# Kernel tuning notes

Hardware: AMD Instinct MI355X
Metric: run time of the kernel (lower is better)

## Reference

```python
import jax, jax.numpy as jnp
import numpy as np

B, C, H, W = 16, 512, 32, 32
MID = max(8, C // 4)      # gate hidden
CA_MID = max(8, C // 4)   # channel-attn hidden
LOW_RADIUS = 0.35


def dct_mat(N):
    # Orthonormal DCT-II matrix: D[k,n] = s_k * sqrt(2/N) * cos(pi*(2n+1)*k/(2N))
    k = jnp.arange(N, dtype=jnp.float32)[:, None]
    n = jnp.arange(N, dtype=jnp.float32)[None, :]
    M = jnp.cos(jnp.pi * (2.0 * n + 1.0) * k / (2.0 * N)) * jnp.sqrt(2.0 / N)
    return M.at[0].multiply(1.0 / jnp.sqrt(2.0))


def build_low_mask(Hh, Ww, low_radius):
    yy = jnp.arange(Hh, dtype=jnp.float32)[:, None] / max(Hh - 1, 1)
    xx = jnp.arange(Ww, dtype=jnp.float32)[None, :] / max(Ww - 1, 1)
    rr = jnp.sqrt(yy ** 2 + xx ** 2)
    rr = rr / jnp.maximum(rr.max(), 1e-6)
    return (rr <= low_radius).astype(jnp.float32)[None, None]  # [1,1,H,W]


def conv1x1(x, w, b):
    # x: [B,Cin,H,W], w: [Cout,Cin], b: [Cout]
    return jnp.einsum('bchw,oc->bohw', x, w) + b[None, :, None, None]


def freq_transform(x, gw1, gb1, gw2, gb2, Dh, Dw, lm):
    # gate: avgpool -> 1x1 -> relu -> 1x1 -> sigmoid, output 2 scalars per sample
    pooled = jnp.mean(x, axis=(2, 3), keepdims=True)  # [B,C,1,1]
    g = jax.nn.sigmoid(conv1x1(jax.nn.relu(conv1x1(pooled, gw1, gb1)), gw2, gb2))
    g_low, g_high = g[:, 0:1], g[:, 1:2]  # [B,1,1,1]
    # 2D ortho DCT: Dh @ x @ Dw^T
    freq = jnp.einsum('ih,bchw->bciw', Dh, x)
    freq = jnp.einsum('jw,bchw->bchj', Dw, freq)
    # frequency gating fused
    gated = freq * (g_low * lm + g_high * (1.0 - lm))
    # inverse: Dh^T @ freq @ Dw
    out = jnp.einsum('hi,bchw->bciw', Dh, gated)
    out = jnp.einsum('wj,bchw->bchj', Dw, out)
    return out


def setup_inputs() -> dict:
    key = jax.random.key(0)
    ks = jax.random.split(key, 24)
    s = 1.0 / np.sqrt(C)
    d = {
        'rgb': jax.random.normal(ks[0], (B, C, H, W), jnp.float32),
        'dsm': jax.random.normal(ks[1], (B, C, H, W), jnp.float32),
        'rgb_w': jax.random.normal(ks[2], (C, C), jnp.float32) * s,
        'rgb_b': jax.random.normal(ks[3], (C,), jnp.float32) * 0.01,
        'dsm_w': jax.random.normal(ks[4], (C, C), jnp.float32) * s,
        'dsm_b': jax.random.normal(ks[5], (C,), jnp.float32) * 0.01,
        'gate_w1': jax.random.normal(ks[6], (MID, C), jnp.float32) * s,
        'gate_b1': jax.random.normal(ks[7], (MID,), jnp.float32) * 0.01,
        'gate_w2': jax.random.normal(ks[8], (2, MID), jnp.float32) * (1.0 / np.sqrt(MID)),
        'gate_b2': jax.random.normal(ks[9], (2,), jnp.float32) * 0.01,
        'q_w': jax.random.normal(ks[10], (C, C), jnp.float32) * s,
        'q_b': jax.random.normal(ks[11], (C,), jnp.float32) * 0.01,
        'k_w': jax.random.normal(ks[12], (C, C), jnp.float32) * s,
        'k_b': jax.random.normal(ks[13], (C,), jnp.float32) * 0.01,
        'v_w': jax.random.normal(ks[14], (C, C), jnp.float32) * s,
        'v_b': jax.random.normal(ks[15], (C,), jnp.float32) * 0.01,
        'sp_w': jax.random.normal(ks[16], (C, C, 3, 3), jnp.float32) * (s / 3.0),
        'sp_b': jax.random.normal(ks[17], (C,), jnp.float32) * 0.01,
        'ca_w1': jax.random.normal(ks[18], (CA_MID, C), jnp.float32) * s,
        'ca_b1': jax.random.normal(ks[19], (CA_MID,), jnp.float32) * 0.01,
        'ca_w2': jax.random.normal(ks[20], (C, CA_MID), jnp.float32) * (1.0 / np.sqrt(CA_MID)),
        'ca_b2': jax.random.normal(ks[21], (C,), jnp.float32) * 0.01,
    }
    return d


def reference(rgb, dsm, rgb_w, rgb_b, dsm_w, dsm_b, gate_w1, gate_b1, gate_w2, gate_b2,
              q_w, q_b, k_w, k_b, v_w, v_b, sp_w, sp_b, ca_w1, ca_b1, ca_w2, ca_b2):
    Dh, Dw = dct_mat(H), dct_mat(W)
    lm = build_low_mask(H, W, LOW_RADIUS)

    rgb_p = conv1x1(rgb, rgb_w, rgb_b)
    dsm_p = conv1x1(dsm, dsm_w, dsm_b)

    rgb_f = freq_transform(rgb_p, gate_w1, gate_b1, gate_w2, gate_b2, Dh, Dw, lm)
    dsm_f = freq_transform(dsm_p, gate_w1, gate_b1, gate_w2, gate_b2, Dh, Dw, lm)

    q = conv1x1(rgb_f, q_w, q_b).reshape(B, C, H * W)
    k = conv1x1(dsm_f, k_w, k_b).reshape(B, C, H * W)
    v = conv1x1(dsm_f, v_w, v_b).reshape(B, C, H * W)

    # attn over spatial tokens: [B,N,N]
    scores = jnp.einsum('bcn,bcm->bnm', q, k) / jnp.sqrt(jnp.float32(C))
    attn = jax.nn.softmax(scores, axis=-1)
    out = jnp.einsum('bnm,bcm->bcn', attn, v).reshape(B, C, H, W)

    spatial = jax.lax.conv_general_dilated(
        out, sp_w, window_strides=(1, 1), padding='SAME',
        dimension_numbers=('NCHW', 'OIHW', 'NCHW')) + sp_b[None, :, None, None]

    pooled = jnp.mean(spatial, axis=(2, 3), keepdims=True)
    weight = jax.nn.sigmoid(conv1x1(jax.nn.relu(conv1x1(pooled, ca_w1, ca_b1)), ca_w2, ca_b2))
    return rgb_p + spatial * weight
```

## Files before the change

### kernel.cpp

```cpp
#include <hip/hip_runtime.h>

typedef long long i64;
typedef unsigned int u32;
typedef unsigned short u16;

#define Bq 16
#define Cq 512
#define Hq 32
#define Wq 32
#define Nq 1024
#define MIDq 128
#define XPBq 591872

typedef __attribute__((ext_vector_type(8))) short bf16x8;
typedef __attribute__((ext_vector_type(4))) float f32x4;

static __device__ __forceinline__ u16 f2bf(float f) {
  u32 u = __float_as_uint(f);
  u = (u + 0x7FFFu + ((u >> 16) & 1u)) >> 16;
  return (u16)u;
}
static __device__ __forceinline__ float bf2f(u16 h) {
  return __uint_as_float(((u32)h) << 16);
}

__global__ __launch_bounds__(256) void k_prep(
    const float* __restrict__ rgb_w, const float* __restrict__ dsm_w,
    const float* __restrict__ q_w, const float* __restrict__ k_w,
    const float* __restrict__ v_w, const float* __restrict__ sp_w,
    u16* __restrict__ rw_h, u16* __restrict__ rw_l,
    u16* __restrict__ dw_h, u16* __restrict__ dw_l,
    u16* __restrict__ qw_h, u16* __restrict__ qw_l,
    u16* __restrict__ kw_h, u16* __restrict__ kw_l,
    u16* __restrict__ vw_h, u16* __restrict__ vw_l,
    u16* __restrict__ w9h, u16* __restrict__ w9l,
    float* __restrict__ Dm, float* __restrict__ lm) {
  int blk = blockIdx.x, tid = threadIdx.x;
  if (blk < 1280) {
    int wi = blk >> 8;
    const float* src = wi == 0 ? rgb_w : wi == 1 ? dsm_w : wi == 2 ? q_w : wi == 3 ? k_w : v_w;
    u16* hi = wi == 0 ? rw_h : wi == 1 ? dw_h : wi == 2 ? qw_h : wi == 3 ? kw_h : vw_h;
    u16* lo = wi == 0 ? rw_l : wi == 1 ? dw_l : wi == 2 ? qw_l : wi == 3 ? kw_l : vw_l;
    i64 idx = ((i64)(blk & 255) * 256 + tid) * 4;
    float4 f = *(const float4*)(src + idx);
    ushort4 h, l;
    h.x = f2bf(f.x); l.x = f2bf(f.x - bf2f(h.x));
    h.y = f2bf(f.y); l.y = f2bf(f.y - bf2f(h.y));
    h.z = f2bf(f.z); l.z = f2bf(f.z - bf2f(h.z));
    h.w = f2bf(f.w); l.w = f2bf(f.w - bf2f(h.w));
    *(ushort4*)(hi + idx) = h;
    *(ushort4*)(lo + idx) = l;
  } else if (blk < 1536) {
    int idx = (blk - 1280) * 256 + tid;
    int o = idx >> 7;
    int c4 = (idx & 127) << 2;
    float vals[4][9];
#pragma unroll
    for (int j = 0; j < 4; j++) {
      const float* wp = sp_w + ((i64)o * Cq + c4 + j) * 9;
#pragma unroll
      for (int t = 0; t < 9; t++) vals[j][t] = wp[t];
    }
#pragma unroll
    for (int t = 0; t < 9; t++) {
      ushort4 h, l;
      h.x = f2bf(vals[0][t]); l.x = f2bf(vals[0][t] - bf2f(h.x));
      h.y = f2bf(vals[1][t]); l.y = f2bf(vals[1][t] - bf2f(h.y));
      h.z = f2bf(vals[2][t]); l.z = f2bf(vals[2][t] - bf2f(h.z));
      h.w = f2bf(vals[3][t]); l.w = f2bf(vals[3][t] - bf2f(h.w));
      i64 od = (i64)t * (Cq * Cq) + (i64)o * Cq + c4;
      *(ushort4*)(w9h + od) = h;
      *(ushort4*)(w9l + od) = l;
    }
  } else {
#pragma unroll
    for (int q4 = 0; q4 < 4; q4++) {
      int t = tid * 4 + q4;
      int i = t >> 5, j = t & 31;
      float v = cosf(3.14159265358979323846f * (2.0f * j + 1.0f) * (float)i / 64.0f) * 0.25f;
      if (i == 0) v *= 0.7071067811865476f;
      Dm[t] = v;
      float yy = i * (1.0f / 31.0f), xx = j * (1.0f / 31.0f);
      float rr = sqrtf(yy * yy + xx * xx) * 0.7071067811865476f;
      lm[t] = (rr <= 0.35f) ? 1.0f : 0.0f;
    }
  }
}

__global__ __launch_bounds__(64) void k_zero_border(u16* __restrict__ xp) {
  int i = blockIdx.x;
  int b = blockIdx.y;
  int arr = blockIdx.z;
  int pr;
  if (i < 34) pr = i;
  else if (i < 68) pr = 33 * 34 + (i - 34);
  else { int j = i - 68; pr = (1 + (j >> 1)) * 34 + (j & 1) * 33; }
  u16* p = xp + (i64)arr * ((i64)Bq * XPBq) + (i64)b * XPBq + (i64)pr * Cq;
  *(uint4*)(p + threadIdx.x * 8) = (uint4){0u, 0u, 0u, 0u};
}

__global__ __launch_bounds__(256) void k_gemm(
    const u16* __restrict__ Ahi, const u16* __restrict__ Alo,
    const float* __restrict__ Af32, int a_mode, i64 sAb,
    const u16* __restrict__ Bhi, const u16* __restrict__ Blo,
    const float* __restrict__ Bf32, int b_mode, i64 sBb,
    const float* __restrict__ bias, int bias_mode, float scale,
    int M, int N, int K,
    float* __restrict__ Cf, u16* __restrict__ Chi, u16* __restrict__ Clo,
    i64 sCb, int out_mode) {
  __shared__ __align__(16) u16 As_h[128][40];
  __shared__ __align__(16) u16 As_l[128][40];
  __shared__ __align__(16) u16 Bs_h[128][40];
  __shared__ __align__(16) u16 Bs_l[128][40];
  int tid = threadIdx.x;
  int gx = gridDim.x, gxy = gx * gridDim.y;
  int nwg = gxy * gridDim.z;
  int orig = blockIdx.x + gx * blockIdx.y + gxy * blockIdx.z;
  int wg = (nwg & 7) ? orig : ((orig & 7) * (nwg >> 3) + (orig >> 3));
  int b = wg / gxy;
  int rem = wg - b * gxy;
  int m0 = (rem / gx) << 7;
  int n0 = (rem - (rem / gx) * gx) << 7;
  const u16* pAhi = Ahi + (i64)b * (a_mode ? 0 : sAb);
  const u16* pAlo = Alo + (i64)b * (a_mode ? 0 : sAb);
  const float* pAf = a_mode ? (Af32 + (i64)b * sAb) : nullptr;
  const u16* pBhi = Bhi + (i64)b * (b_mode ? 0 : sBb);
  const u16* pBlo = Blo + (i64)b * (b_mode ? 0 : sBb);
  const float* pBf = b_mode ? (Bf32 + (i64)b * sBb) : nullptr;
  int lane = tid & 63;
  int wid = tid >> 6;
  int wm = (wid & 1) << 6;
  int wn = (wid >> 1) << 6;
  int l15 = lane & 15;
  int g8 = (lane >> 4) << 3;
  f32x4 acc[4][4];
#pragma unroll
  for (int mi = 0; mi < 4; mi++)
#pragma unroll
    for (int nj = 0; nj < 4; nj++)
      acc[mi][nj] = (f32x4){0.f, 0.f, 0.f, 0.f};

  for (int k0 = 0; k0 < K; k0 += 32) {
    if (a_mode == 0) {
#pragma unroll
      for (int i = 0; i < 4; i++) {
        int r = ((i & 1) << 6) + (tid >> 2);
        int seg = tid & 3;
        const u16* src = (i < 2) ? pAhi : pAlo;
        uint4 val = *(const uint4*)(src + (i64)(m0 + r) * K + k0 + seg * 8);
        if (i < 2) *(uint4*)&As_h[r][seg * 8] = val;
        else       *(uint4*)&As_l[r][seg * 8] = val;
      }
    } else {
      int cs = tid >> 6, ns = tid & 63;
      const float* src = pAf + (i64)(k0 + cs * 8) * M + m0 + ns * 2;
      float2 f[8];
#pragma unroll
      for (int j = 0; j < 8; j++) f[j] = *(const float2*)(src + (i64)j * M);
#pragma unroll
      for (int i = 0; i < 2; i++) {
        union { u16 u[8]; uint4 v; } hh, ll;
#pragma unroll
        for (int j = 0; j < 8; j++) {
          float x = i ? f[j].y : f[j].x;
          u16 h = f2bf(x);
          hh.u[j] = h;
          ll.u[j] = (u16)(__float_as_uint(x - bf2f(h)) >> 16);
        }
        *(uint4*)&As_h[2 * ns + i][8 * cs] = hh.v;
        *(uint4*)&As_l[2 * ns + i][8 * cs] = ll.v;
      }
    }
    if (b_mode == 0) {
#pragma unroll
      for (int i = 0; i < 4; i++) {
        int r = ((i & 1) << 6) + (tid >> 2);
        int seg = tid & 3;
        const u16* src = (i < 2) ? pBhi : pBlo;
        uint4 val = *(const uint4*)(src + (i64)(n0 + r) * K + k0 + seg * 8);
        if (i < 2) *(uint4*)&Bs_h[r][seg * 8] = val;
        else       *(uint4*)&Bs_l[r][seg * 8] = val;
      }
    } else {
      int cs = tid >> 6, ns = tid & 63;
      const float* src = pBf + (i64)(k0 + cs * 8) * N + n0 + ns * 2;
      float2 f[8];
#pragma unroll
      for (int j = 0; j < 8; j++) f[j] = *(const float2*)(src + (i64)j * N);
#pragma unroll
      for (int i = 0; i < 2; i++) {
        union { u16 u[8]; uint4 v; } hh, ll;
#pragma unroll
        for (int j = 0; j < 8; j++) {
          float x = i ? f[j].y : f[j].x;
          u16 h = f2bf(x);
          hh.u[j] = h;
          ll.u[j] = (u16)(__float_as_uint(x - bf2f(h)) >> 16);
        }
        *(uint4*)&Bs_h[2 * ns + i][8 * cs] = hh.v;
        *(uint4*)&Bs_l[2 * ns + i][8 * cs] = ll.v;
      }
    }
    __syncthreads();
    bf16x8 ah[4], al[4], bh[4], bl[4];
#pragma unroll
    for (int mi = 0; mi < 4; mi++) {
      int row = wm + mi * 16 + l15;
      ah[mi] = *(const bf16x8*)&As_h[row][g8];
      al[mi] = *(const bf16x8*)&As_l[row][g8];
    }
#pragma unroll
    for (int nj = 0; nj < 4; nj++) {
      int row = wn + nj * 16 + l15;
      bh[nj] = *(const bf16x8*)&Bs_h[row][g8];
      bl[nj] = *(const bf16x8*)&Bs_l[row][g8];
    }
#pragma unroll
    for (int mi = 0; mi < 4; mi++)
#pragma unroll
      for (int nj = 0; nj < 4; nj++) {
        acc[mi][nj] = __builtin_amdgcn_mfma_f32_16x16x32_bf16(ah[mi], bh[nj], acc[mi][nj], 0, 0, 0);
        acc[mi][nj] = __builtin_amdgcn_mfma_f32_16x16x32_bf16(ah[mi], bl[nj], acc[mi][nj], 0, 0, 0);
        acc[mi][nj] = __builtin_amdgcn_mfma_f32_16x16x32_bf16(al[mi], bh[nj], acc[mi][nj], 0, 0, 0);
      }
    __syncthreads();
  }

#pragma unroll
  for (int mi = 0; mi < 4; mi++)
#pragma unroll
    for (int nj = 0; nj < 4; nj++) {
      int col_g = n0 + wn + nj * 16 + l15;
      int row_b = m0 + wm + mi * 16 + ((lane >> 4) << 2);
      float v4[4];
#pragma unroll
      for (int r = 0; r < 4; r++) {
        float val = acc[mi][nj][r] * scale;
        if (bias_mode == 1) val += bias[row_b + r];
        else if (bias_mode == 2) val += bias[col_g];
        v4[r] = val;
      }
      if (out_mode == 0) {
#pragma unroll
        for (int r = 0; r < 4; r++)
          Cf[(i64)b * sCb + (i64)(row_b + r) * N + col_g] = v4[r];
      } else if (out_mode == 1) {
#pragma unroll
        for (int r = 0; r < 4; r++) {
          i64 o = (i64)b * sCb + (i64)(row_b + r) * N + col_g;
          u16 h = f2bf(v4[r]);
          Chi[o] = h;
          Clo[o] = f2bf(v4[r] - bf2f(h));
        }
      } else {
        int pr = ((col_g >> 5) + 1) * 34 + (col_g & 31) + 1;
        i64 o = (i64)b * sCb + (i64)pr * Cq + row_b;
        ushort4 hh, ll;
        hh.x = f2bf(v4[0]); ll.x = f2bf(v4[0] - bf2f(hh.x));
        hh.y = f2bf(v4[1]); ll.y = f2bf(v4[1] - bf2f(hh.y));
        hh.z = f2bf(v4[2]); ll.z = f2bf(v4[2] - bf2f(hh.z));
        hh.w = f2bf(v4[3]); ll.w = f2bf(v4[3] - bf2f(hh.w));
        *(ushort4*)(Chi + o) = hh;
        *(ushort4*)(Clo + o) = ll;
      }
    }
}

__global__ __launch_bounds__(256) void k_conv3_mfma(
    const u16* __restrict__ Wh, const u16* __restrict__ Wl,
    const u16* __restrict__ Xh, const u16* __restrict__ Xl,
    const float* __restrict__ bias, float* __restrict__ out) {
  __shared__ __align__(16) u16 As_h[128][72];
  __shared__ __align__(16) u16 As_l[128][72];
  __shared__ __align__(16) u16 Bs_h[128][72];
  __shared__ __align__(16) u16 Bs_l[128][72];
  int tid = threadIdx.x;
  int gx = gridDim.x, gxy = gx * gridDim.y;
  int nwg = gxy * gridDim.z;
  int orig = blockIdx.x + gx * blockIdx.y + gxy * blockIdx.z;
  int wg = (nwg & 7) ? orig : ((orig & 7) * (nwg >> 3) + (orig >> 3));
  int b = wg / gxy;
  int rem = wg - b * gxy;
  int m0 = (rem / gx) << 7;
  int n0 = (rem - (rem / gx) * gx) << 7;
  const u16* pXh = Xh + (i64)b * XPBq;
  const u16* pXl = Xl + (i64)b * XPBq;
  int lane = tid & 63;
  int wid = tid >> 6;
  int wm = (wid & 1) << 6;
  int wn = (wid >> 1) << 6;
  int l15 = lane & 15;
  int g8 = (lane >> 4) << 3;
  int rr = tid >> 2, seg = tid & 3;
  int n_a = n0 + rr, n_b = n0 + 64 + rr;
  int prb0 = (n_a >> 5) * 34 + (n_a & 31);
  int prb1 = (n_b >> 5) * 34 + (n_b & 31);
  f32x4 acc[4][4];
#pragma unroll
  for (int mi = 0; mi < 4; mi++)
#pragma unroll
    for (int nj = 0; nj < 4; nj++)
      acc[mi][nj] = (f32x4){0.f, 0.f, 0.f, 0.f};

  for (int tap = 0; tap < 9; tap++) {
    int doff = (tap / 3) * 34 + (tap % 3);
    const u16* wth = Wh + (i64)tap * (Cq * Cq);
    const u16* wtl = Wl + (i64)tap * (Cq * Cq);
    i64 bb0 = (i64)(prb0 + doff) * Cq;
    i64 bb1 = (i64)(prb1 + doff) * Cq;
    for (int c0 = 0; c0 < Cq; c0 += 64) {
#pragma unroll
      for (int half = 0; half < 2; half++) {
        int col = seg * 8 + half * 32;
        i64 gc = c0 + col;
        *(uint4*)&As_h[rr][col]      = *(const uint4*)(wth + (i64)(m0 + rr) * Cq + gc);
        *(uint4*)&As_h[64 + rr][col] = *(const uint4*)(wth + (i64)(m0 + 64 + rr) * Cq + gc);
        *(uint4*)&As_l[rr][col]      = *(const uint4*)(wtl + (i64)(m0 + rr) * Cq + gc);
        *(uint4*)&As_l[64 + rr][col] = *(const uint4*)(wtl + (i64)(m0 + 64 + rr) * Cq + gc);
        *(uint4*)&Bs_h[rr][col]      = *(const uint4*)(pXh + bb0 + gc);
        *(uint4*)&Bs_h[64 + rr][col] = *(const uint4*)(pXh + bb1 + gc);
        *(uint4*)&Bs_l[rr][col]      = *(const uint4*)(pXl + bb0 + gc);
        *(uint4*)&Bs_l[64 + rr][col] = *(const uint4*)(pXl + bb1 + gc);
      }
      __syncthreads();
#pragma unroll
      for (int ks = 0; ks < 2; ks++) {
        int gk = ks * 32 + g8;
        bf16x8 ah[4], al[4], bh[4], bl[4];
#pragma unroll
        for (int mi = 0; mi < 4; mi++) {
          int row = wm + mi * 16 + l15;
          ah[mi] = *(const bf16x8*)&As_h[row][gk];
          al[mi] = *(const bf16x8*)&As_l[row][gk];
        }
#pragma unroll
        for (int nj = 0; nj < 4; nj++) {
          int row = wn + nj * 16 + l15;
          bh[nj] = *(const bf16x8*)&Bs_h[row][gk];
          bl[nj] = *(const bf16x8*)&Bs_l[row][gk];
        }
#pragma unroll
        for (int mi = 0; mi < 4; mi++)
#pragma unroll
          for (int nj = 0; nj < 4; nj++) {
            acc[mi][nj] = __builtin_amdgcn_mfma_f32_16x16x32_bf16(ah[mi], bh[nj], acc[mi][nj], 0, 0, 0);
            acc[mi][nj] = __builtin_amdgcn_mfma_f32_16x16x32_bf16(ah[mi], bl[nj], acc[mi][nj], 0, 0, 0);
            acc[mi][nj] = __builtin_amdgcn_mfma_f32_16x16x32_bf16(al[mi], bh[nj], acc[mi][nj], 0, 0, 0);
          }
      }
      __syncthreads();
    }
  }

#pragma unroll
  for (int mi = 0; mi < 4; mi++)
#pragma unroll
    for (int nj = 0; nj < 4; nj++) {
      int col_g = n0 + wn + nj * 16 + l15;
#pragma unroll
      for (int r = 0; r < 4; r++) {
        int row_g = m0 + wm + mi * 16 + ((lane >> 4) << 2) + r;
        float val = acc[mi][nj][r] + bias[row_g];
        out[(i64)b * (Cq * Nq) + (i64)row_g * Nq + col_g] = val;
      }
    }
}

__global__ __launch_bounds__(256) void k_pool(const float* __restrict__ x, float* __restrict__ o) {
  int gw = (int)((blockIdx.x * 256 + threadIdx.x) >> 6);
  int ln = threadIdx.x & 63;
  const float* p = x + (i64)gw * Nq;
  float s = 0.f;
#pragma unroll
  for (int it = 0; it < 4; it++) {
    float4 v = *(const float4*)(p + ln * 4 + it * 256);
    s += v.x + v.y + v.z + v.w;
  }
#pragma unroll
  for (int off = 32; off > 0; off >>= 1) s += __shfl_xor(s, off, 64);
  if (ln == 0) o[gw] = s * (1.0f / 1024.0f);
}

__global__ __launch_bounds__(128) void k_gate(
    const float* __restrict__ pooled, const float* __restrict__ w1,
    const float* __restrict__ b1, const float* __restrict__ w2,
    const float* __restrict__ b2, float* __restrict__ g) {
  __shared__ float pl[Cq];
  __shared__ float h[MIDq];
  int bb = blockIdx.x, tid = threadIdx.x;
  for (int c = tid; c < Cq; c += 128) pl[c] = pooled[bb * Cq + c];
  __syncthreads();
  float s = b1[tid];
  const float* wr = w1 + (i64)tid * Cq;
  for (int c = 0; c < Cq; c++) s = fmaf(wr[c], pl[c], s);
  h[tid] = fmaxf(s, 0.f);
  __syncthreads();
  if (tid < 2) {
    float t = b2[tid];
    const float* w2r = w2 + tid * MIDq;
    for (int m = 0; m < MIDq; m++) t = fmaf(w2r[m], h[m], t);
    g[bb * 2 + tid] = 1.0f / (1.0f + expf(-t));
  }
}

__global__ __launch_bounds__(256) void k_freq(
    const float* __restrict__ xr, const float* __restrict__ xd,
    float* __restrict__ yr, float* __restrict__ yd,
    const float* __restrict__ g_r, const float* __restrict__ g_d,
    const float* __restrict__ Dm, const float* __restrict__ lm) {
  __shared__ float Ds[32][36], Dt[32][36], Xs[32][36], T1[32][36];
  int bid = blockIdx.x;
  const float* x; float* y; const float* g;
  if (bid < Bq * Cq) {
    x = xr + (i64)bid * Nq; y = yr + (i64)bid * Nq; g = g_r + (bid >> 9) * 2;
  } else {
    int id = bid - Bq * Cq;
    x = xd + (i64)id * Nq; y = yd + (i64)id * Nq; g = g_d + (id >> 9) * 2;
  }
  int tid = threadIdx.x;
  int r_ = tid >> 3, j4 = (tid & 7) << 2;
  {
    float4 dv = *(const float4*)(Dm + tid * 4);
    *(float4*)&Ds[r_][j4] = dv;
    Dt[j4 + 0][r_] = dv.x; Dt[j4 + 1][r_] = dv.y;
    Dt[j4 + 2][r_] = dv.z; Dt[j4 + 3][r_] = dv.w;
    *(float4*)&Xs[r_][j4] = *(const float4*)(x + tid * 4);
  }
  float gl = g[0], gh = g[1];
  __syncthreads();
  float a0 = 0, a1 = 0, a2 = 0, a3 = 0;
#pragma unroll
  for (int h = 0; h < 32; h++) {
    float a = Ds[r_][h];
    float4 bv = *(const float4*)&Xs[h][j4];
    a0 = fmaf(a, bv.x, a0); a1 = fmaf(a, bv.y, a1);
    a2 = fmaf(a, bv.z, a2); a3 = fmaf(a, bv.w, a3);
  }
  *(float4*)&T1[r_][j4] = make_float4(a0, a1, a2, a3);
  __syncthreads();
  a0 = a1 = a2 = a3 = 0;
#pragma unroll
  for (int w = 0; w < 32; w++) {
    float a = T1[r_][w];
    float4 bv = *(const float4*)&Dt[w][j4];
    a0 = fmaf(a, bv.x, a0); a1 = fmaf(a, bv.y, a1);
    a2 = fmaf(a, bv.z, a2); a3 = fmaf(a, bv.w, a3);
  }
  {
    float4 mv = *(const float4*)(lm + r_ * 32 + j4);
    a0 *= fmaf(gl, mv.x, gh * (1.f - mv.x));
    a1 *= fmaf(gl, mv.y, gh * (1.f - mv.y));
    a2 *= fmaf(gl, mv.z, gh * (1.f - mv.z));
    a3 *= fmaf(gl, mv.w, gh * (1.f - mv.w));
  }
  __syncthreads();
  *(float4*)&Xs[r_][j4] = make_float4(a0, a1, a2, a3);
  __syncthreads();
  a0 = a1 = a2 = a3 = 0;
#pragma unroll
  for (int ii = 0; ii < 32; ii++) {
    float a = Dt[r_][ii];
    float4 bv = *(const float4*)&Xs[ii][j4];
    a0 = fmaf(a, bv.x, a0); a1 = fmaf(a, bv.y, a1);
    a2 = fmaf(a, bv.z, a2); a3 = fmaf(a, bv.w, a3);
  }
  __syncthreads();
  *(float4*)&T1[r_][j4] = make_float4(a0, a1, a2, a3);
  __syncthreads();
  a0 = a1 = a2 = a3 = 0;
#pragma unroll
  for (int jj = 0; jj < 32; jj++) {
    float a = T1[r_][jj];
    float4 bv = *(const float4*)&Ds[jj][j4];
    a0 = fmaf(a, bv.x, a0); a1 = fmaf(a, bv.y, a1);
    a2 = fmaf(a, bv.z, a2); a3 = fmaf(a, bv.w, a3);
  }
  *(float4*)(y + tid * 4) = make_float4(a0, a1, a2, a3);
}

__global__ __launch_bounds__(256) void k_softmax_split(
    const float* __restrict__ sc, u16* __restrict__ ahi, u16* __restrict__ alo) {
  __shared__ float redm[4], reds[4];
  i64 row = blockIdx.x;
  const float* p = sc + row * (i64)Nq;
  int tid = threadIdx.x;
  float4 v = ((const float4*)p)[tid];
  float mx = fmaxf(fmaxf(v.x, v.y), fmaxf(v.z, v.w));
#pragma unroll
  for (int o = 32; o > 0; o >>= 1) mx = fmaxf(mx, __shfl_xor(mx, o, 64));
  if ((tid & 63) == 0) redm[tid >> 6] = mx;
  __syncthreads();
  mx = fmaxf(fmaxf(redm[0], redm[1]), fmaxf(redm[2], redm[3]));
  v.x = expf(v.x - mx); v.y = expf(v.y - mx);
  v.z = expf(v.z - mx); v.w = expf(v.w - mx);
  float s = v.x + v.y + v.z + v.w;
#pragma unroll
  for (int o = 32; o > 0; o >>= 1) s += __shfl_xor(s, o, 64);
  if ((tid & 63) == 0) reds[tid >> 6] = s;
  __syncthreads();
  s = reds[0] + reds[1] + reds[2] + reds[3];
  float inv = 1.0f / s;
  v.x *= inv; v.y *= inv; v.z *= inv; v.w *= inv;
  ushort4 h, l;
  h.x = f2bf(v.x); l.x = f2bf(v.x - bf2f(h.x));
  h.y = f2bf(v.y); l.y = f2bf(v.y - bf2f(h.y));
  h.z = f2bf(v.z); l.z = f2bf(v.z - bf2f(h.z));
  h.w = f2bf(v.w); l.w = f2bf(v.w - bf2f(h.w));
  *(ushort4*)(ahi + row * Nq + tid * 4) = h;
  *(ushort4*)(alo + row * Nq + tid * 4) = l;
}

__global__ __launch_bounds__(512) void k_ca(
    const float* __restrict__ pooled, const float* __restrict__ w1,
    const float* __restrict__ b1, const float* __restrict__ w2,
    const float* __restrict__ b2, float* __restrict__ wt) {
  __shared__ float pl[Cq];
  __shared__ float h[MIDq];
  int b = blockIdx.x, tid = threadIdx.x;
  pl[tid] = pooled[b * Cq + tid];
  __syncthreads();
  if (tid < MIDq) {
    float s = b1[tid];
    const float* wr = w1 + (i64)tid * Cq;
    for (int c = 0; c < Cq; c++) s = fmaf(wr[c], pl[c], s);
    h[tid] = fmaxf(s, 0.f);
  }
  __syncthreads();
  float s = b2[tid];
  const float* wr = w2 + (i64)tid * MIDq;
  for (int m = 0; m < MIDq; m++) s = fmaf(wr[m], h[m], s);
  wt[b * Cq + tid] = 1.0f / (1.0f + expf(-s));
}

__global__ __launch_bounds__(256) void k_final(
    const float* __restrict__ rgbp, const float* __restrict__ sp,
    const float* __restrict__ wt, float* __restrict__ out) {
  i64 idx = (i64)blockIdx.x * 256 + threadIdx.x;
  float4 a = ((const float4*)rgbp)[idx];
  float4 s = ((const float4*)sp)[idx];
  float w = wt[idx >> 8];
  float4 r;
  r.x = fmaf(s.x, w, a.x); r.y = fmaf(s.y, w, a.y);
  r.z = fmaf(s.z, w, a.z); r.w = fmaf(s.w, w, a.w);
  ((float4*)out)[idx] = r;
}

extern "C" void kernel_launch(void* const* d_in, const int* in_sizes, int n_in,
                              void* d_out, int out_size, void* d_ws, size_t ws_size,
                              hipStream_t stream) {
  (void)in_sizes; (void)n_in; (void)out_size; (void)ws_size;
  const float* rgb    = (const float*)d_in[0];
  const float* dsm    = (const float*)d_in[1];
  const float* rgb_w  = (const float*)d_in[2];
  const float* rgb_b  = (const float*)d_in[3];
  const float* dsm_w  = (const float*)d_in[4];
  const float* dsm_b  = (const float*)d_in[5];
  const float* gate_w1 = (const float*)d_in[6];
  const float* gate_b1 = (const float*)d_in[7];
  const float* gate_w2 = (const float*)d_in[8];
  const float* gate_b2 = (const float*)d_in[9];
  const float* q_w = (const float*)d_in[10];
  const float* q_b = (const float*)d_in[11];
  const float* k_w = (const float*)d_in[12];
  const float* k_b = (const float*)d_in[13];
  const float* v_w = (const float*)d_in[14];
  const float* v_b = (const float*)d_in[15];
  const float* sp_w = (const float*)d_in[16];
  const float* sp_b = (const float*)d_in[17];
  const float* ca_w1 = (const float*)d_in[18];
  const float* ca_b1 = (const float*)d_in[19];
  const float* ca_w2 = (const float*)d_in[20];
  const float* ca_b2 = (const float*)d_in[21];

  const i64 S  = (i64)Bq * Cq * Nq;
  const i64 SU = S;
  const i64 WE = (i64)Cq * Cq;
  const i64 XPT = (i64)Bq * XPBq;

  float* wsf = (float*)d_ws;
  float* rgbp   = wsf;
  float* dsmp   = wsf + S;
  float* rgbf   = wsf + 2 * S;
  float* dsmf   = wsf + 3 * S;
  float* scores  = dsmp;
  float* spatial = dsmf;
  u16* XPh = (u16*)dsmp;
  u16* XPl = XPh + XPT;
  float* smallr = wsf + 4 * S;
  float* Dm     = smallr;
  float* lm     = smallr + 1024;
  float* pooled = smallr + 2048;
  float* g_all  = smallr + 18432;
  float* wt     = smallr + 18496;
  u16* ub = (u16*)(wsf + 4 * S + 32768);
  u16* U0 = ub;          u16* U1 = ub + SU;
  u16* U2 = ub + 2 * SU;
  u16* U4 = ub + 4 * SU; u16* U5 = ub + 5 * SU;
  u16* wb = ub + 6 * SU;
  u16* rgbw_h = wb;           u16* rgbw_l = wb + WE;
  u16* dsmw_h = wb + 2 * WE;  u16* dsmw_l = wb + 3 * WE;
  u16* qw_h   = wb + 4 * WE;  u16* qw_l   = wb + 5 * WE;
  u16* kw_h   = wb + 6 * WE;  u16* kw_l   = wb + 7 * WE;
  u16* vw_h   = wb + 8 * WE;  u16* vw_l   = wb + 9 * WE;
  u16* w9h    = wb + 10 * WE; u16* w9l    = wb + 19 * WE;

  const i64 sT = (i64)Nq * Cq;
  const i64 sS = (i64)Nq * Nq;
  const float rsqc = 0.044194173824159216f;

  k_prep<<<1537, 256, 0, stream>>>(rgb_w, dsm_w, q_w, k_w, v_w, sp_w,
                                   rgbw_h, rgbw_l, dsmw_h, dsmw_l, qw_h, qw_l,
                                   kw_h, kw_l, vw_h, vw_l, w9h, w9l, Dm, lm);

  dim3 gW(Nq / 128, Cq / 128, Bq);
  dim3 gQ(Cq / 128, Nq / 128, Bq);
  dim3 gS(Nq / 128, Nq / 128, Bq);

  k_gemm<<<gW, 256, 0, stream>>>(rgbw_h, rgbw_l, nullptr, 0, 0,
                                 nullptr, nullptr, rgb, 1, sT,
                                 rgb_b, 1, 1.0f, Cq, Nq, Cq,
                                 rgbp, nullptr, nullptr, sT, 0);
  k_gemm<<<gW, 256, 0, stream>>>(dsmw_h, dsmw_l, nullptr, 0, 0,
                                 nullptr, nullptr, dsm, 1, sT,
                                 dsm_b, 1, 1.0f, Cq, Nq, Cq,
                                 dsmp, nullptr, nullptr, sT, 0);

  k_pool<<<(2 * Bq * Cq) / 4, 256, 0, stream>>>(rgbp, pooled);
  k_gate<<<32, 128, 0, stream>>>(pooled, gate_w1, gate_b1, gate_w2, gate_b2, g_all);

  k_freq<<<2 * Bq * Cq, 256, 0, stream>>>(rgbp, dsmp, rgbf, dsmf, g_all, g_all + 32, Dm, lm);

  k_gemm<<<gQ, 256, 0, stream>>>(nullptr, nullptr, rgbf, 1, sT,
                                 qw_h, qw_l, nullptr, 0, 0,
                                 q_b, 2, 1.0f, Nq, Cq, Cq,
                                 nullptr, U4, U5, sT, 1);
  k_gemm<<<gQ, 256, 0, stream>>>(nullptr, nullptr, dsmf, 1, sT,
                                 kw_h, kw_l, nullptr, 0, 0,
                                 k_b, 2, 1.0f, Nq, Cq, Cq,
                                 nullptr, U0, U1, sT, 1);
  k_gemm<<<gS, 256, 0, stream>>>(U4, U5, nullptr, 0, sT,
                                 U0, U1, nullptr, 0, sT,
                                 nullptr, 0, rsqc, Nq, Nq, Cq,
                                 scores, nullptr, nullptr, sS, 0);
  k_gemm<<<gW, 256, 0, stream>>>(vw_h, vw_l, nullptr, 0, 0,
                                 nullptr, nullptr, dsmf, 1, sT,
                                 v_b, 1, 1.0f, Cq, Nq, Cq,
                                 nullptr, U4, U5, sT, 1);
  k_softmax_split<<<Bq * Nq, 256, 0, stream>>>(scores, U0, U2);
  k_zero_border<<<dim3(132, Bq, 2), 64, 0, stream>>>(XPh);
  k_gemm<<<gW, 256, 0, stream>>>(U4, U5, nullptr, 0, sT,
                                 U0, U2, nullptr, 0, sS,
                                 nullptr, 0, 1.0f, Cq, Nq, Nq,
                                 nullptr, XPh, XPl, XPBq, 2);

  k_conv3_mfma<<<dim3(Nq / 128, Cq / 128, Bq), 256, 0, stream>>>(
      w9h, w9l, XPh, XPl, sp_b, spatial);

  k_pool<<<(Bq * Cq) / 4, 256, 0, stream>>>(spatial, pooled);
  k_ca<<<Bq, 512, 0, stream>>>(pooled, ca_w1, ca_b1, ca_w2, ca_b2, wt);

  k_final<<<(int)(S / 4 / 256), 256, 0, stream>>>(rgbp, spatial, wt, (float*)d_out);
}
```

Baseline: 758.9 us.

## Reuse halo input tile across all nine conv taps in shared memory

The 3x3 conv GEMM now loads a padded halo block of input rows (6 padded image rows, 204 positions) into shared memory once per 32-channel chunk. It then iterates all nine taps by offsetting into that tile, instead of re-reading shifted input from global memory for every tap. This cuts global input traffic by about 9x at the cost of 2.6x more staged rows. The K chunk shrinks from 64 to 32, so there are more syncs per MFMA. The unpadded 32-wide LDS rows may also cause bank conflicts.

```diff
diff --git a/kernel.cpp b/kernel.cpp
--- a/kernel.cpp
+++ b/kernel.cpp
@@ -270,10 +270,10 @@
     const u16* __restrict__ Wh, const u16* __restrict__ Wl,
     const u16* __restrict__ Xh, const u16* __restrict__ Xl,
     const float* __restrict__ bias, float* __restrict__ out) {
-  __shared__ __align__(16) u16 As_h[128][72];
-  __shared__ __align__(16) u16 As_l[128][72];
-  __shared__ __align__(16) u16 Bs_h[128][72];
-  __shared__ __align__(16) u16 Bs_l[128][72];
+  __shared__ __align__(16) u16 As_h[128][32];
+  __shared__ __align__(16) u16 As_l[128][32];
+  __shared__ __align__(16) u16 Bs_h[204][32];
+  __shared__ __align__(16) u16 Bs_l[204][32];
   int tid = threadIdx.x;
   int gx = gridDim.x, gxy = gx * gridDim.y;
   int nwg = gxy * gridDim.z;
@@ -283,18 +283,21 @@
   int rem = wg - b * gxy;
   int m0 = (rem / gx) << 7;
   int n0 = (rem - (rem / gx) * gx) << 7;
-  const u16* pXh = Xh + (i64)b * XPBq;
-  const u16* pXl = Xl + (i64)b * XPBq;
   int lane = tid & 63;
   int wid = tid >> 6;
   int wm = (wid & 1) << 6;
   int wn = (wid >> 1) << 6;
   int l15 = lane & 15;
   int g8 = (lane >> 4) << 3;
-  int rr = tid >> 2, seg = tid & 3;
-  int n_a = n0 + rr, n_b = n0 + 64 + rr;
-  int prb0 = (n_a >> 5) * 34 + (n_a & 31);
-  int prb1 = (n_b >> 5) * 34 + (n_b & 31);
+  int yb = n0 >> 5;
+  const u16* pXh = Xh + (i64)b * XPBq + (i64)(yb * 34) * Cq;
+  const u16* pXl = Xl + (i64)b * XPBq + (i64)(yb * 34) * Cq;
+  int bbase[4];
+#pragma unroll
+  for (int nj = 0; nj < 4; nj++) {
+    int nloc = wn + nj * 16 + l15;
+    bbase[nj] = (nloc >> 5) * 34 + (nloc & 31);
+  }
   f32x4 acc[4][4];
 #pragma unroll
   for (int mi = 0; mi < 4; mi++)
@@ -302,52 +305,45 @@
     for (int nj = 0; nj < 4; nj++)
       acc[mi][nj] = (f32x4){0.f, 0.f, 0.f, 0.f};
 
-  for (int tap = 0; tap < 9; tap++) {
-    int doff = (tap / 3) * 34 + (tap % 3);
-    const u16* wth = Wh + (i64)tap * (Cq * Cq);
-    const u16* wtl = Wl + (i64)tap * (Cq * Cq);
-    i64 bb0 = (i64)(prb0 + doff) * Cq;
-    i64 bb1 = (i64)(prb1 + doff) * Cq;
-    for (int c0 = 0; c0 < Cq; c0 += 64) {
-#pragma unroll
-      for (int half = 0; half < 2; half++) {
-        int col = seg * 8 + half * 32;
-        i64 gc = c0 + col;
-        *(uint4*)&As_h[rr][col]      = *(const uint4*)(wth + (i64)(m0 + rr) * Cq + gc);
-        *(uint4*)&As_h[64 + rr][col] = *(const uint4*)(wth + (i64)(m0 + 64 + rr) * Cq + gc);
-        *(uint4*)&As_l[rr][col]      = *(const uint4*)(wtl + (i64)(m0 + rr) * Cq + gc);
-        *(uint4*)&As_l[64 + rr][col] = *(const uint4*)(wtl + (i64)(m0 + 64 + rr) * Cq + gc);
-        *(uint4*)&Bs_h[rr][col]      = *(const uint4*)(pXh + bb0 + gc);
-        *(uint4*)&Bs_h[64 + rr][col] = *(const uint4*)(pXh + bb1 + gc);
-        *(uint4*)&Bs_l[rr][col]      = *(const uint4*)(pXl + bb0 + gc);
-        *(uint4*)&Bs_l[64 + rr][col] = *(const uint4*)(pXl + bb1 + gc);
+  for (int c0 = 0; c0 < Cq; c0 += 32) {
+    for (int e = tid; e < 816; e += 256) {
+      int row = e >> 2, q = e & 3;
+      i64 src = (i64)row * Cq + c0 + q * 8;
+      *(uint4*)&Bs_h[row][q * 8] = *(const uint4*)(pXh + src);
+      *(uint4*)&Bs_l[row][q * 8] = *(const uint4*)(pXl + src);
+    }
+    for (int tap = 0; tap < 9; tap++) {
+      int doff = (tap / 3) * 34 + (tap % 3);
+      {
+        int r = tid >> 1, q0 = (tid & 1) << 1;
+        i64 wo = (i64)tap * (Cq * Cq) + (i64)(m0 + r) * Cq + c0;
+        *(uint4*)&As_h[r][q0 * 8]       = *(const uint4*)(Wh + wo + q0 * 8);
+        *(uint4*)&As_h[r][(q0 + 1) * 8] = *(const uint4*)(Wh + wo + (q0 + 1) * 8);
+        *(uint4*)&As_l[r][q0 * 8]       = *(const uint4*)(Wl + wo + q0 * 8);
+        *(uint4*)&As_l[r][(q0 + 1) * 8] = *(const uint4*)(Wl + wo + (q0 + 1) * 8);
       }
       __syncthreads();
-#pragma unroll
-      for (int ks = 0; ks < 2; ks++) {
-        int gk = ks * 32 + g8;
-        bf16x8 ah[4], al[4], bh[4], bl[4];
-#pragma unroll
-        for (int mi = 0; mi < 4; mi++) {
-          int row = wm + mi * 16 + l15;
-          ah[mi] = *(const bf16x8*)&As_h[row][gk];
-          al[mi] = *(const bf16x8*)&As_l[row][gk];
+      bf16x8 ah[4], al[4], bh[4], bl[4];
+#pragma unroll
+      for (int mi = 0; mi < 4; mi++) {
+        int row = wm + mi * 16 + l15;
+        ah[mi] = *(const bf16x8*)&As_h[row][g8];
+        al[mi] = *(const bf16x8*)&As_l[row][g8];
+      }
+#pragma unroll
+      for (int nj = 0; nj < 4; nj++) {
+        int row = bbase[nj] + doff;
+        bh[nj] = *(const bf16x8*)&Bs_h[row][g8];
+        bl[nj] = *(const bf16x8*)&Bs_l[row][g8];
+      }
+#pragma unroll
+      for (int mi = 0; mi < 4; mi++)
+#pragma unroll
+        for (int nj = 0; nj < 4; nj++) {
+          acc[mi][nj] = __builtin_amdgcn_mfma_f32_16x16x32_bf16(ah[mi], bh[nj], acc[mi][nj], 0, 0, 0);
+          acc[mi][nj] = __builtin_amdgcn_mfma_f32_16x16x32_bf16(ah[mi], bl[nj], acc[mi][nj], 0, 0, 0);
+          acc[mi][nj] = __builtin_amdgcn_mfma_f32_16x16x32_bf16(al[mi], bh[nj], acc[mi][nj], 0, 0, 0);
         }
-#pragma unroll
-        for (int nj = 0; nj < 4; nj++) {
-          int row = wn + nj * 16 + l15;
-          bh[nj] = *(const bf16x8*)&Bs_h[row][gk];
-          bl[nj] = *(const bf16x8*)&Bs_l[row][gk];
-        }
-#pragma unroll
-        for (int mi = 0; mi < 4; mi++)
-#pragma unroll
-          for (int nj = 0; nj < 4; nj++) {
-            acc[mi][nj] = __builtin_amdgcn_mfma_f32_16x16x32_bf16(ah[mi], bh[nj], acc[mi][nj], 0, 0, 0);
-            acc[mi][nj] = __builtin_amdgcn_mfma_f32_16x16x32_bf16(ah[mi], bl[nj], acc[mi][nj], 0, 0, 0);
-            acc[mi][nj] = __builtin_amdgcn_mfma_f32_16x16x32_bf16(al[mi], bh[nj], acc[mi][nj], 0, 0, 0);
-          }
-      }
       __syncthreads();
     }
   }
```

Measured after the change: 735.6 us. 1.03x faster.
